# Optimization experiments

Hardware: AMD Instinct MI355X
Metric: run time of the kernel (lower is better)

Reference implementation:

```python
import jax, jax.numpy as jnp
import numpy as np

SEQ = 8192
DIM = 1024

def setup_inputs() -> dict:
    key = jax.random.key(0)
    kx, kq, kk, kv1, kv2 = jax.random.split(key, 5)
    std = 0.01  # flax nn.initializers.normal() default stddev=1e-2
    return {
        "x": jax.random.normal(kx, (SEQ, DIM), dtype=jnp.float32),
        "wq": jax.random.normal(kq, (DIM, DIM), dtype=jnp.float32) * std,
        "wk": jax.random.normal(kk, (DIM, DIM), dtype=jnp.float32) * std,
        "wv1": jax.random.normal(kv1, (DIM, DIM), dtype=jnp.float32) * std,
        "wv2": jax.random.normal(kv2, (DIM, DIM), dtype=jnp.float32) * std,
    }

def reference(x, wq, wk, wv1, wv2):
    # x: [S, D]; single-head causal self-attention with SiLU-gated output proj
    q = x @ wq              # [S, D]
    k = x @ wk              # [S, D]
    v = x @ wv1             # [S, D]
    dim_head = q.shape[-1]
    dots = (q @ k.T) * (dim_head ** -0.5)          # [S, S]
    s = x.shape[-2]
    mask = jnp.tril(jnp.ones((s, s), dtype=bool))
    dots = jnp.where(mask, dots, -1e9)
    attn = jax.nn.softmax(dots, axis=-1)            # [S, S]
    hidden = attn @ v                               # [S, D]
    return jax.nn.silu(hidden) @ wv2                # [S, D]
```

## Files before the change

### kernel.cpp

```cpp
#include <hip/hip_runtime.h>
#include <hip/hip_bf16.h>
#include <cstdint>
#include <cstddef>

constexpr int SEQ = 8192;
constexpr int DIM = 1024;
constexpr int BAND = 2048;

typedef __attribute__((ext_vector_type(8))) short short8;
typedef __attribute__((ext_vector_type(4))) float f32x4;
typedef __attribute__((ext_vector_type(4))) unsigned short us4;

#define MFMA_BF16 __builtin_amdgcn_mfma_f32_16x16x32_bf16

static __device__ __forceinline__ unsigned short f2bf(float f) {
    uint32_t u = __builtin_bit_cast(uint32_t, f);
    u += 0x7FFFu + ((u >> 16) & 1u);
    return (unsigned short)(u >> 16);
}
static __device__ __forceinline__ float bf2f(unsigned short h) {
    uint32_t u = ((uint32_t)h) << 16;
    return __builtin_bit_cast(float, u);
}
static __device__ __forceinline__ int r64(int x) {
    return ((x + 32) >> 6) << 6;
}

#define GLOAD16(gp, lp) __builtin_amdgcn_global_load_lds(                      \
    (const __attribute__((address_space(1))) void*)(gp),                       \
    (__attribute__((address_space(3))) void*)(lp), 16, 0, 0)

template<int OM, bool CAUSAL, bool KCAP, bool SPLITK>
__global__ __launch_bounds__(256, 4)
void gemm_bt(const unsigned short* __restrict__ A,
             const unsigned short* __restrict__ Bt,
             void* __restrict__ Cp,
             int M, int N, int K, float scale, int rowBase, int NS,
             float* __restrict__ Sp)
{
    constexpr int BM = 128, BK = 64, BN = 128;
    constexpr int NF = BN / 32;
    __shared__ __align__(16) unsigned short As[BM * BK];
    __shared__ __align__(16) unsigned short Bs[BN * BK];

    const int t = threadIdx.x;
    const int lane = t & 63, w = t >> 6;
    const int wr = w >> 1, wc = w & 1;
    const int ln15 = lane & 15, hi = lane >> 4;

    const int gx = gridDim.x, gy = gridDim.y;
    const int nwg = gx * gy * gridDim.z;
    const int orig = blockIdx.y + gy * (blockIdx.x + gx * blockIdx.z);
    const int q = nwg >> 3, r8 = nwg & 7;
    const int xcd = orig & 7, idx = orig >> 3;
    const int wg = (xcd < r8 ? xcd * (q + 1)
                             : r8 * (q + 1) + (xcd - r8) * q) + idx;
    const int byi = wg % gy, tmpw = wg / gy;
    const int bxi = tmpw % gx, bzi = tmpw / gx;

    const int bm = byi * BM, bn = bxi * BN;

    if (CAUSAL && bn > rowBase + bm + (BM - 1)) return;
    int Keff = K;
    if (KCAP) { int kc = rowBase + bm + BM; Keff = kc < K ? kc : K; }
    int kbeg = 0, kend = Keff;
    if (SPLITK) {
        kbeg = r64(bzi * Keff / NS);
        int ke = r64((bzi + 1) * Keff / NS);
        kend = ke < Keff ? ke : Keff;
        if (kbeg >= kend) return;
    }

    f32x4 acc[4][NF] = {};

    for (int k0 = kbeg; k0 < kend; k0 += BK) {
        #pragma unroll
        for (int i = 0; i < 4; ++i) {
            int c = t + 256 * i;
            int r = c >> 3, qq = (c & 7) ^ (r & 7);
            GLOAD16(A + (size_t)(bm + r) * K + k0 + qq * 8, As + c * 8);
        }
        #pragma unroll
        for (int i = 0; i < 4; ++i) {
            int c = t + 256 * i;
            int r = c >> 3, qq = (c & 7) ^ (r & 7);
            GLOAD16(Bt + (size_t)(bn + r) * K + k0 + qq * 8, Bs + c * 8);
        }
        __syncthreads();

        #pragma unroll
        for (int kk = 0; kk < 2; ++kk) {
            short8 a[4], b[NF];
            #pragma unroll
            for (int m = 0; m < 4; ++m) {
                int r = wr * 64 + m * 16 + ln15;
                int s = (kk * 4 + hi) ^ (r & 7);
                a[m] = *(const short8*)(As + r * 64 + s * 8);
            }
            #pragma unroll
            for (int n = 0; n < NF; ++n) {
                int r = wc * 64 + n * 16 + ln15;
                int s = (kk * 4 + hi) ^ (r & 7);
                b[n] = *(const short8*)(Bs + r * 64 + s * 8);
            }
            __builtin_amdgcn_s_setprio(1);
            #pragma unroll
            for (int m = 0; m < 4; ++m)
                #pragma unroll
                for (int n = 0; n < NF; ++n)
                    acc[m][n] = MFMA_BF16(a[m], b[n], acc[m][n], 0, 0, 0);
            __builtin_amdgcn_s_setprio(0);
        }
        __syncthreads();
    }

    if (OM == 5) {
        float psum[4][4];
        #pragma unroll
        for (int m = 0; m < 4; ++m)
            #pragma unroll
            for (int j = 0; j < 4; ++j) {
                int row = bm + wr * 64 + m * 16 + hi * 4 + j;
                int grow = rowBase + row;
                float s = 0.f;
                #pragma unroll
                for (int n = 0; n < NF; ++n) {
                    int col = bn + wc * 64 + n * 16 + ln15;
                    float p = (col <= grow)
                        ? __expf(acc[m][n][j] * scale) : 0.f;
                    ((unsigned short*)Cp)[(size_t)row * N + col] = f2bf(p);
                    s += p;
                }
                psum[m][j] = s;
            }
        #pragma unroll
        for (int off = 1; off < 16; off <<= 1)
            #pragma unroll
            for (int m = 0; m < 4; ++m)
                #pragma unroll
                for (int j = 0; j < 4; ++j)
                    psum[m][j] += __shfl_xor(psum[m][j], off, 64);
        if (ln15 == 0) {
            const int ci = bxi * 2 + wc;
            #pragma unroll
            for (int m = 0; m < 4; ++m)
                #pragma unroll
                for (int j = 0; j < 4; ++j)
                    Sp[(size_t)(bm + wr * 64 + m * 16 + hi * 4 + j) * 128 + ci]
                        = psum[m][j];
        }
        return;
    }
    #pragma unroll
    for (int m = 0; m < 4; ++m)
        #pragma unroll
        for (int n = 0; n < NF; ++n)
            #pragma unroll
            for (int j = 0; j < 4; ++j) {
                int row = bm + wr * 64 + m * 16 + hi * 4 + j;
                int col = bn + wc * 64 + n * 16 + ln15;
                float v = acc[m][n][j] * scale;
                if (OM == 0)
                    ((unsigned short*)Cp)[(size_t)row * N + col] = f2bf(v);
                else if (OM == 2)
                    ((float*)Cp)[(size_t)row * N + col] = v;
                else if (OM == 3)
                    ((unsigned short*)Cp + (size_t)bzi * M * N)
                        [(size_t)row * N + col] = f2bf(v);
                else {
                    unsigned short* qb = (unsigned short*)Cp;
                    if (col < DIM)
                        qb[(size_t)row * DIM + col] = f2bf(v);
                    else if (col < 2 * DIM)
                        (qb + (size_t)SEQ * DIM)
                            [(size_t)row * DIM + (col - DIM)] = f2bf(v);
                    else
                        (qb + (size_t)2 * SEQ * DIM)
                            [(size_t)(col - 2 * DIM) * SEQ + row] = f2bf(v);
                }
            }
}

__global__ __launch_bounds__(256)
void reduce_silu(const unsigned short* __restrict__ part,
                 const float* __restrict__ Sp,
                 unsigned short* __restrict__ out, int ns, int rowBase)
{
    __shared__ float red[4];
    const int t = threadIdx.x, lane = t & 63, w = t >> 6;
    const size_t idx = ((size_t)blockIdx.x * 256 + t) * 8;
    const int r = (int)(idx >> 10);
    int keb = rowBase + ((r >> 7) << 7) + 128;
    if (keb > SEQ) keb = SEQ;

    {
        const int rloc = blockIdx.x * 2 + (t >> 7);
        const int seg = t & 127;
        const int nct = 2 * (((rowBase + rloc) >> 7) + 1);
        float val = (seg < nct) ? Sp[(size_t)rloc * 128 + seg] : 0.f;
        #pragma unroll
        for (int off = 1; off < 64; off <<= 1)
            val += __shfl_xor(val, off, 64);
        if (lane == 0) red[w] = val;
    }
    __syncthreads();
    const float inv = 1.0f /
        ((t < 128) ? (red[0] + red[1]) : (red[2] + red[3]));

    float s[8] = {};
    for (int z = 0; z < ns; ++z) {
        int b0 = r64(z * keb / ns);
        int b1 = r64((z + 1) * keb / ns);
        if (b1 > keb) b1 = keb;
        if (b1 > b0) {
            short8 p = *(const short8*)(part + (size_t)z * (BAND * DIM) + idx);
            #pragma unroll
            for (int j = 0; j < 8; ++j) s[j] += bf2f((unsigned short)p[j]);
        }
    }
    short8 o;
    #pragma unroll
    for (int j = 0; j < 8; ++j) {
        float v = s[j] * inv;
        o[j] = (short)f2bf(v / (1.0f + __expf(-v)));
    }
    *(short8*)(out + idx) = o;
}

__global__ __launch_bounds__(256)
void cvt_bf16(const float* __restrict__ X, unsigned short* __restrict__ Y)
{
    int i = (blockIdx.x * 256 + threadIdx.x) * 8;
    f32x4 v0 = *(const f32x4*)(X + i);
    f32x4 v1 = *(const f32x4*)(X + i + 4);
    short8 o = { (short)f2bf(v0[0]), (short)f2bf(v0[1]),
                 (short)f2bf(v0[2]), (short)f2bf(v0[3]),
                 (short)f2bf(v1[0]), (short)f2bf(v1[1]),
                 (short)f2bf(v1[2]), (short)f2bf(v1[3]) };
    *(short8*)(Y + i) = o;
}

__global__ __launch_bounds__(256)
void twT(const float* __restrict__ W, unsigned short* __restrict__ WT)
{
    __shared__ float tile[64][65];
    const int bx = blockIdx.x * 64, by = blockIdx.y * 64;
    const int t = threadIdx.x, rr = t >> 4, c4 = (t & 15) * 4;
    #pragma unroll
    for (int i = 0; i < 4; ++i) {
        int r = rr + i * 16;
        f32x4 v = *(const f32x4*)(W + (size_t)(by + r) * DIM + bx + c4);
        tile[r][c4 + 0] = v[0]; tile[r][c4 + 1] = v[1];
        tile[r][c4 + 2] = v[2]; tile[r][c4 + 3] = v[3];
    }
    __syncthreads();
    #pragma unroll
    for (int i = 0; i < 4; ++i) {
        int r = rr + i * 16;
        us4 o = { f2bf(tile[c4 + 0][r]), f2bf(tile[c4 + 1][r]),
                  f2bf(tile[c4 + 2][r]), f2bf(tile[c4 + 3][r]) };
        *(us4*)(WT + (size_t)(bx + r) * DIM + by + c4) = o;
    }
}

extern "C" void kernel_launch(void* const* d_in, const int* in_sizes, int n_in,
                              void* d_out, int out_size, void* d_ws, size_t ws_size,
                              hipStream_t stream)
{
    const float* x   = (const float*)d_in[0];
    const float* wq  = (const float*)d_in[1];
    const float* wk  = (const float*)d_in[2];
    const float* wv1 = (const float*)d_in[3];
    const float* wv2 = (const float*)d_in[4];

    const size_t E = (size_t)SEQ * DIM;
    unsigned short* qbuf  = (unsigned short*)d_ws;
    unsigned short* kbuf  = qbuf + E;
    unsigned short* vtbuf = kbuf + E;
    unsigned short* part  = vtbuf + E;
    float* Sp = (float*)(part + 4 * (size_t)BAND * DIM);
    const size_t PBUF = (size_t)BAND * DIM * sizeof(unsigned short);
    int nsplit = 1;
    if (ws_size >= 3 * E * sizeof(unsigned short) + 4 * PBUF
                   + 128 * (size_t)BAND * sizeof(float)) nsplit = 4;

    unsigned short* xb    = (unsigned short*)d_out;
    unsigned short* wqkv  = xb + E;
    unsigned short* Sband = (unsigned short*)d_out;

    dim3 tg(16, 16);
    cvt_bf16<<<SEQ * DIM / 2048, 256, 0, stream>>>(x, xb);
    twT<<<tg, 256, 0, stream>>>(wq,  wqkv);
    twT<<<tg, 256, 0, stream>>>(wk,  wqkv + DIM * DIM);
    twT<<<tg, 256, 0, stream>>>(wv1, wqkv + 2 * DIM * DIM);

    gemm_bt<4,false,false,false><<<dim3(3 * DIM / 128, SEQ / 128), 256, 0, stream>>>(
        xb, wqkv, qbuf, SEQ, 3 * DIM, DIM, 1.0f, 0, 0, nullptr);

    for (int b = 0; b < 4; ++b) {
        const int rb = b * BAND;
        const int ncol = (rb + BAND) / 128;
        dim3 gq(ncol, BAND / 128);
        gemm_bt<5,true,false,false><<<gq, 256, 0, stream>>>(
            qbuf + (size_t)rb * DIM, kbuf, Sband, BAND, SEQ, DIM,
            0.03125f, rb, 0, Sp);
        if (b == 3)
            twT<<<tg, 256, 0, stream>>>(wv2, kbuf);
        dim3 gpv(DIM / 128, BAND / 128, nsplit);
        gemm_bt<3,false,true,true><<<gpv, 256, 0, stream>>>(
            Sband, vtbuf, part, BAND, DIM, SEQ, 1.0f, rb, nsplit, nullptr);
        reduce_silu<<<BAND * DIM / 2048, 256, 0, stream>>>(
            part, Sp, qbuf + (size_t)rb * DIM, nsplit, rb);
    }

    gemm_bt<2,false,false,false><<<dim3(DIM / 128, SEQ / 128), 256, 0, stream>>>(
        qbuf, kbuf, d_out, SEQ, DIM, DIM, 1.0f, 0, 0, nullptr);
}
```

Before: 366.9 us.

## Use larger 4096-row attention bands in workspace and batch weight transposes

When the workspace is large enough, the score band buffer moves from the output buffer into the workspace and grows from 2048 to 4096 rows. The attention loop then runs two bands instead of four, so it issues fewer kernel launches and each GEMM gets a larger grid. The three QKV weight transposes are merged into one launch that uses a z-dimension. This needs more workspace memory, and the larger grids may change load balance across the causal bands.

```diff
diff --git a/kernel.cpp b/kernel.cpp
--- a/kernel.cpp
+++ b/kernel.cpp
@@ -5,7 +5,6 @@
 
 constexpr int SEQ = 8192;
 constexpr int DIM = 1024;
-constexpr int BAND = 2048;
 
 typedef __attribute__((ext_vector_type(8))) short short8;
 typedef __attribute__((ext_vector_type(4))) float f32x4;
@@ -184,7 +183,7 @@
 __global__ __launch_bounds__(256)
 void reduce_silu(const unsigned short* __restrict__ part,
                  const float* __restrict__ Sp,
-                 unsigned short* __restrict__ out, int ns, int rowBase)
+                 unsigned short* __restrict__ out, int ns, int rowBase, int bsz)
 {
     __shared__ float red[4];
     const int t = threadIdx.x, lane = t & 63, w = t >> 6;
@@ -213,7 +212,7 @@
         int b1 = r64((z + 1) * keb / ns);
         if (b1 > keb) b1 = keb;
         if (b1 > b0) {
-            short8 p = *(const short8*)(part + (size_t)z * (BAND * DIM) + idx);
+            short8 p = *(const short8*)(part + (size_t)z * bsz * DIM + idx);
             #pragma unroll
             for (int j = 0; j < 8; ++j) s[j] += bf2f((unsigned short)p[j]);
         }
@@ -240,8 +239,8 @@
     *(short8*)(Y + i) = o;
 }
 
-__global__ __launch_bounds__(256)
-void twT(const float* __restrict__ W, unsigned short* __restrict__ WT)
+static __device__ __forceinline__ void twT_body(
+    const float* __restrict__ W, unsigned short* __restrict__ WT)
 {
     __shared__ float tile[64][65];
     const int bx = blockIdx.x * 64, by = blockIdx.y * 64;
@@ -263,6 +262,20 @@
     }
 }
 
+__global__ __launch_bounds__(256)
+void twT(const float* __restrict__ W, unsigned short* __restrict__ WT)
+{
+    twT_body(W, WT);
+}
+
+__global__ __launch_bounds__(256)
+void twT3(const float* __restrict__ W0, const float* __restrict__ W1,
+          const float* __restrict__ W2, unsigned short* __restrict__ WT)
+{
+    const float* W = (blockIdx.z == 0) ? W0 : (blockIdx.z == 1) ? W1 : W2;
+    twT_body(W, WT + (size_t)blockIdx.z * DIM * DIM);
+}
+
 extern "C" void kernel_launch(void* const* d_in, const int* in_sizes, int n_in,
                               void* d_out, int out_size, void* d_ws, size_t ws_size,
                               hipStream_t stream)
@@ -277,40 +290,52 @@
     unsigned short* qbuf  = (unsigned short*)d_ws;
     unsigned short* kbuf  = qbuf + E;
     unsigned short* vtbuf = kbuf + E;
-    unsigned short* part  = vtbuf + E;
-    float* Sp = (float*)(part + 4 * (size_t)BAND * DIM);
-    const size_t PBUF = (size_t)BAND * DIM * sizeof(unsigned short);
-    int nsplit = 1;
-    if (ws_size >= 3 * E * sizeof(unsigned short) + 4 * PBUF
-                   + 128 * (size_t)BAND * sizeof(float)) nsplit = 4;
+    unsigned short* wsfree = vtbuf + E;
+    const size_t avail = ws_size - 3 * E * sizeof(unsigned short);
 
     unsigned short* xb    = (unsigned short*)d_out;
     unsigned short* wqkv  = xb + E;
-    unsigned short* Sband = (unsigned short*)d_out;
-
-    dim3 tg(16, 16);
+
+    int bandsz;
+    unsigned short *Sband, *part;
+    float* Sp;
+    int nsplit = 4;
+    const size_t need4096 = (size_t)4096 * SEQ * 2
+                          + (size_t)4 * 4096 * DIM * 2
+                          + (size_t)4096 * 128 * 4;
+    if (avail >= need4096) {
+        bandsz = 4096;
+        Sband  = wsfree;
+        part   = Sband + (size_t)4096 * SEQ;
+        Sp     = (float*)(part + (size_t)4 * 4096 * DIM);
+    } else {
+        bandsz = 2048;
+        Sband  = (unsigned short*)d_out;
+        part   = wsfree;
+        Sp     = (float*)(part + (size_t)4 * 2048 * DIM);
+        if (avail < (size_t)4 * 2048 * DIM * 2 + (size_t)2048 * 128 * 4)
+            nsplit = 1;
+    }
+
     cvt_bf16<<<SEQ * DIM / 2048, 256, 0, stream>>>(x, xb);
-    twT<<<tg, 256, 0, stream>>>(wq,  wqkv);
-    twT<<<tg, 256, 0, stream>>>(wk,  wqkv + DIM * DIM);
-    twT<<<tg, 256, 0, stream>>>(wv1, wqkv + 2 * DIM * DIM);
+    twT3<<<dim3(16, 16, 3), 256, 0, stream>>>(wq, wk, wv1, wqkv);
 
     gemm_bt<4,false,false,false><<<dim3(3 * DIM / 128, SEQ / 128), 256, 0, stream>>>(
         xb, wqkv, qbuf, SEQ, 3 * DIM, DIM, 1.0f, 0, 0, nullptr);
 
-    for (int b = 0; b < 4; ++b) {
-        const int rb = b * BAND;
-        const int ncol = (rb + BAND) / 128;
-        dim3 gq(ncol, BAND / 128);
+    for (int rb = 0; rb < SEQ; rb += bandsz) {
+        const int ncol = (rb + bandsz) / 128;
+        dim3 gq(ncol, bandsz / 128);
         gemm_bt<5,true,false,false><<<gq, 256, 0, stream>>>(
-            qbuf + (size_t)rb * DIM, kbuf, Sband, BAND, SEQ, DIM,
+            qbuf + (size_t)rb * DIM, kbuf, Sband, bandsz, SEQ, DIM,
             0.03125f, rb, 0, Sp);
-        if (b == 3)
-            twT<<<tg, 256, 0, stream>>>(wv2, kbuf);
-        dim3 gpv(DIM / 128, BAND / 128, nsplit);
+        if (rb + bandsz == SEQ)
+            twT<<<dim3(16, 16), 256, 0, stream>>>(wv2, kbuf);
+        dim3 gpv(DIM / 128, bandsz / 128, nsplit);
         gemm_bt<3,false,true,true><<<gpv, 256, 0, stream>>>(
-            Sband, vtbuf, part, BAND, DIM, SEQ, 1.0f, rb, nsplit, nullptr);
-        reduce_silu<<<BAND * DIM / 2048, 256, 0, stream>>>(
-            part, Sp, qbuf + (size_t)rb * DIM, nsplit, rb);
+            Sband, vtbuf, part, bandsz, DIM, SEQ, 1.0f, rb, nsplit, nullptr);
+        reduce_silu<<<bandsz * DIM / 2048, 256, 0, stream>>>(
+            part, Sp, qbuf + (size_t)rb * DIM, nsplit, rb, bandsz);
     }
 
     gemm_bt<2,false,false,false><<<dim3(DIM / 128, SEQ / 128), 256, 0, stream>>>(
```

Measured after the change: 347.1 us (median of 3 runs). -5.4%, faster.
